# Kernel optimization log

Measured on AMD Instinct MI355X. Metric: run time of the kernel, lower is better.

## Reference

```python
import jax, jax.numpy as jnp
import numpy as np

V, E, HD, B, L, T = 50000, 512, 1024, 64, 512, 16
H = HD // 2
START, STOP = 14, 15
NEG = -10000.0


def setup_inputs() -> dict:
    key = jax.random.key(0)
    ks = jax.random.split(key, 14)
    def n(k, shape, s=0.1):
        return jax.random.normal(k, shape, dtype=jnp.float32) * s
    sentences = jax.random.randint(ks[0], (B, L), 0, V)
    embed = n(ks[1], (V, E), 1.0)
    Wih_f = n(ks[2], (4 * H, E)); Whh_f = n(ks[3], (4 * H, H)); b_f = n(ks[4], (4 * H,))
    Wih_b = n(ks[5], (4 * H, E)); Whh_b = n(ks[6], (4 * H, H)); b_b = n(ks[7], (4 * H,))
    h0 = n(ks[8], (2, B, H), 1.0)  # torch init_hidden uses randn
    c0 = n(ks[9], (2, B, H), 1.0)
    W_tag = n(ks[10], (T, HD)); b_tag = n(ks[11], (T,))
    transitions = jax.random.normal(ks[12], (T, T), dtype=jnp.float32)
    transitions = transitions.at[START, :].set(NEG).at[:, STOP].set(NEG)
    return dict(sentences=sentences, embed=embed, Wih_f=Wih_f, Whh_f=Whh_f, b_f=b_f,
                Wih_b=Wih_b, Whh_b=Whh_b, b_b=b_b, h0=h0, c0=c0,
                W_tag=W_tag, b_tag=b_tag, transitions=transitions)


def _lstm_dir(x, h0, c0, Wih, Whh, b, reverse):
    # x: [L, B, E]; torch gate order i, f, g, o
    def step(carry, xt):
        h, c = carry
        g = xt @ Wih.T + h @ Whh.T + b  # [B, 4H]
        i, f, gg, o = jnp.split(g, 4, axis=-1)
        c = jax.nn.sigmoid(f) * c + jax.nn.sigmoid(i) * jnp.tanh(gg)
        h = jax.nn.sigmoid(o) * jnp.tanh(c)
        return (h, c), h
    _, hs = jax.lax.scan(step, (h0, c0), x, reverse=reverse)
    return hs  # [L, B, H], outputs in original time order


def _viterbi(feats, transitions):
    # feats: [L, T]. Vectorized tag recurrence: fuse matrix-broadcast + max/argmax per step.
    init = jnp.full((T,), NEG, dtype=feats.dtype).at[START].set(0.0)
    def step(fv, feat):
        scores = fv[None, :] + transitions  # [next_tag, prev_tag]
        return jnp.max(scores, axis=1) + feat, jnp.argmax(scores, axis=1)
    fv, bps = jax.lax.scan(step, init, feats)
    term = fv + transitions[STOP]
    best = jnp.argmax(term)
    def back(tag, bp):
        return bp[tag], tag
    _, path = jax.lax.scan(back, best, bps, reverse=True)
    return term[best], path


def reference(sentences, embed, Wih_f, Whh_f, b_f, Wih_b, Whh_b, b_b, h0, c0, W_tag, b_tag, transitions):
    x = embed[sentences]                      # [B, L, E]
    xt = jnp.transpose(x, (1, 0, 2))          # [L, B, E]
    hf = _lstm_dir(xt, h0[0], c0[0], Wih_f, Whh_f, b_f, False)
    hb = _lstm_dir(xt, h0[1], c0[1], Wih_b, Whh_b, b_b, True)
    hs = jnp.concatenate([hf, hb], axis=-1)   # [L, B, HD]
    feats = jnp.einsum('lbh,th->lbt', hs, W_tag) + b_tag  # [L, B, T]
    feats = jnp.transpose(feats, (1, 0, 2))   # [B, L, T]
    scores, paths = jax.vmap(lambda f: _viterbi(f, transitions))(feats)
    return scores, paths
```

## Files before the change

kernel.cpp:

```cpp
#include <hip/hip_runtime.h>
#include <cstddef>

#define LL 512
#define BB 64
#define EE 512
#define HH 512
#define TT 16
#define START_TAG 14
#define STOP_TAG 15
#define NBLK_DIR 64u

__device__ __forceinline__ unsigned short f2bf(float f) {
  unsigned u = __builtin_bit_cast(unsigned, f);
  unsigned r = u + 0x7FFFu + ((u >> 16) & 1u);
  return (unsigned short)(r >> 16);
}

template <typename XT> __device__ __forceinline__ float ldx(const XT* p);
template <> __device__ __forceinline__ float ldx<float>(const float* p) { return *p; }
template <> __device__ __forceinline__ float ldx<unsigned short>(const unsigned short* p) {
  return __builtin_bit_cast(float, (unsigned)(*p) << 16);
}
template <typename XT> __device__ __forceinline__ void stx(XT* p, float v);
template <> __device__ __forceinline__ void stx<float>(float* p, float v) { *p = v; }
template <> __device__ __forceinline__ void stx<unsigned short>(unsigned short* p, float v) { *p = f2bf(v); }

#define AP 132

template <typename XT>
__global__ __launch_bounds__(256) void gemm_xp(
    const int* __restrict__ sent, const float* __restrict__ embed,
    const float* __restrict__ Wf, const float* __restrict__ Wb,
    const float* __restrict__ bf, const float* __restrict__ bb,
    XT* __restrict__ XPf, XT* __restrict__ XPb)
{
  __shared__ float Al[16 * AP];
  __shared__ float Bl[16 * AP];
  __shared__ int tok[128];

  const int bid = blockIdx.x;
  const int mt = bid & 255;
  const int nt = bid >> 8;
  const int m0 = mt << 7;
  const int n0g = nt << 7;
  const int dir = n0g >> 11;
  const int n0 = n0g & 2047;
  const float* W = dir ? Wb : Wf;
  const float* bias = dir ? bb : bf;
  XT* XP = dir ? XPb : XPf;
  const int tid = threadIdx.x;

  if (tid < 128) {
    int m = m0 + tid;
    int l = m >> 6, b = m & 63;
    tok[tid] = sent[b * LL + l];
  }
  __syncthreads();

  float acc[8][8];
#pragma unroll
  for (int i = 0; i < 8; ++i)
#pragma unroll
    for (int j = 0; j < 8; ++j) acc[i][j] = 0.f;

  const int ty = tid >> 4, tx = tid & 15;

#pragma unroll 1
  for (int k0 = 0; k0 < EE; k0 += 16) {
    __syncthreads();
    for (int i = tid; i < 512; i += 256) {
      int row = i >> 2, q = i & 3;
      float4 va = *(const float4*)(embed + (size_t)tok[row] * EE + k0 + q * 4);
      Al[(q * 4 + 0) * AP + row] = va.x;
      Al[(q * 4 + 1) * AP + row] = va.y;
      Al[(q * 4 + 2) * AP + row] = va.z;
      Al[(q * 4 + 3) * AP + row] = va.w;
      float4 vb = *(const float4*)(W + (size_t)(n0 + row) * EE + k0 + q * 4);
      Bl[(q * 4 + 0) * AP + row] = vb.x;
      Bl[(q * 4 + 1) * AP + row] = vb.y;
      Bl[(q * 4 + 2) * AP + row] = vb.z;
      Bl[(q * 4 + 3) * AP + row] = vb.w;
    }
    __syncthreads();
#pragma unroll
    for (int kk = 0; kk < 16; ++kk) {
      float4 a0 = *(const float4*)(Al + kk * AP + ty * 8);
      float4 a1 = *(const float4*)(Al + kk * AP + ty * 8 + 4);
      float4 b0 = *(const float4*)(Bl + kk * AP + tx * 8);
      float4 b1 = *(const float4*)(Bl + kk * AP + tx * 8 + 4);
      float av[8] = {a0.x, a0.y, a0.z, a0.w, a1.x, a1.y, a1.z, a1.w};
      float bv[8] = {b0.x, b0.y, b0.z, b0.w, b1.x, b1.y, b1.z, b1.w};
#pragma unroll
      for (int i = 0; i < 8; ++i)
#pragma unroll
        for (int j = 0; j < 8; ++j) acc[i][j] = fmaf(av[i], bv[j], acc[i][j]);
    }
  }

  float bval[8];
#pragma unroll
  for (int j = 0; j < 8; ++j) bval[j] = bias[n0 + tx * 8 + j];

#pragma unroll
  for (int i = 0; i < 8; ++i) {
    const int m = m0 + ty * 8 + i;
    const int t = m >> 6, b = m & 63;
#pragma unroll
    for (int j = 0; j < 8; ++j) {
      const int n = n0 + tx * 8 + j;
      const int col = n & 511, g = n >> 9;
      stx<XT>(XP + (((size_t)t * HH + col) * 4 + g) * BB + b, acc[i][j] + bval[j]);
    }
  }
}

__device__ __forceinline__ void dir_barrier(unsigned* cnt, unsigned* rel,
                                            unsigned phase) {
  __syncthreads();
  if (threadIdx.x == 0) {
    __threadfence();
    unsigned old = __hip_atomic_fetch_add(cnt, 1u, __ATOMIC_RELAXED,
                                          __HIP_MEMORY_SCOPE_AGENT);
    if (old == phase * NBLK_DIR - 1u) {
      __hip_atomic_store(rel, phase, __ATOMIC_RELEASE, __HIP_MEMORY_SCOPE_AGENT);
    } else {
      while (__hip_atomic_load(rel, __ATOMIC_ACQUIRE, __HIP_MEMORY_SCOPE_AGENT) < phase)
        __builtin_amdgcn_s_sleep(2);
    }
    __threadfence();
  }
  __syncthreads();
}

template <typename XT>
__global__ __launch_bounds__(512) void lstm_rec(
    const XT* __restrict__ XPTf, const XT* __restrict__ XPTb,
    const float* __restrict__ Whh_f, const float* __restrict__ Whh_b,
    const float* __restrict__ h0, const float* __restrict__ c0,
    float* __restrict__ hbuf,
    float* __restrict__ hs,
    unsigned* __restrict__ bar)
{
  const int bid = blockIdx.x;
  const int dir = bid >> 6;
  const int blk = bid & 63;
  const int tid = threadIdx.x;
  const int wv = __builtin_amdgcn_readfirstlane(tid >> 6);
  const int lane = tid & 63;
  const int col = (blk << 3) + wv;

  const float* Whh = dir ? Whh_b : Whh_f;
  const XT* XP = dir ? XPTb : XPTf;
  float* hA = hbuf + (size_t)dir * (2 * HH * BB);
  float* hB = hA + HH * BB;
  unsigned* cnt = bar + (dir ? 32 : 0);
  unsigned* rel = bar + (dir ? 96 : 64);

  const float* W0 = Whh + ((size_t)0 * HH + col) * HH;
  const float* W1 = Whh + ((size_t)1 * HH + col) * HH;
  const float* W2 = Whh + ((size_t)2 * HH + col) * HH;
  const float* W3 = Whh + ((size_t)3 * HH + col) * HH;

  float creg = c0[(size_t)dir * BB * HH + (size_t)lane * HH + col];
  hA[col * BB + lane] = h0[(size_t)dir * BB * HH + (size_t)lane * HH + col];

  unsigned phase = 1;
  dir_barrier(cnt, rel, phase++);

#pragma unroll 1
  for (int step = 0; step < LL; ++step) {
    const int t = dir ? (LL - 1 - step) : step;
    const float* hcur = (step & 1) ? hB : hA;
    float* hnxt = (step & 1) ? hA : hB;

    const XT* xpp = XP + ((size_t)t * HH + col) * 4 * BB + lane;
    const float xp0 = ldx<XT>(xpp);
    const float xp1 = ldx<XT>(xpp + BB);
    const float xp2 = ldx<XT>(xpp + 2 * BB);
    const float xp3 = ldx<XT>(xpp + 3 * BB);

    float a0 = 0.f, a1 = 0.f, a2 = 0.f, a3 = 0.f;
#pragma unroll 4
    for (int k4 = 0; k4 < HH; k4 += 4) {
      const float4 w0 = *(const float4*)(W0 + k4);
      const float4 w1 = *(const float4*)(W1 + k4);
      const float4 w2 = *(const float4*)(W2 + k4);
      const float4 w3 = *(const float4*)(W3 + k4);
      const float hk0 = hcur[(k4 + 0) * BB + lane];
      const float hk1 = hcur[(k4 + 1) * BB + lane];
      const float hk2 = hcur[(k4 + 2) * BB + lane];
      const float hk3 = hcur[(k4 + 3) * BB + lane];
      a0 = fmaf(hk0, w0.x, a0); a1 = fmaf(hk0, w1.x, a1);
      a2 = fmaf(hk0, w2.x, a2); a3 = fmaf(hk0, w3.x, a3);
      a0 = fmaf(hk1, w0.y, a0); a1 = fmaf(hk1, w1.y, a1);
      a2 = fmaf(hk1, w2.y, a2); a3 = fmaf(hk1, w3.y, a3);
      a0 = fmaf(hk2, w0.z, a0); a1 = fmaf(hk2, w1.z, a1);
      a2 = fmaf(hk2, w2.z, a2); a3 = fmaf(hk2, w3.z, a3);
      a0 = fmaf(hk3, w0.w, a0); a1 = fmaf(hk3, w1.w, a1);
      a2 = fmaf(hk3, w2.w, a2); a3 = fmaf(hk3, w3.w, a3);
    }

    const float ig = 1.f / (1.f + expf(-(xp0 + a0)));
    const float fg = 1.f / (1.f + expf(-(xp1 + a1)));
    const float gg = tanhf(xp2 + a2);
    const float og = 1.f / (1.f + expf(-(xp3 + a3)));
    creg = fg * creg + ig * gg;
    const float hv = og * tanhf(creg);

    hnxt[col * BB + lane] = hv;
    hs[((size_t)t * BB + lane) * 1024 + dir * HH + col] = hv;

    dir_barrier(cnt, rel, phase++);
  }
}

__global__ __launch_bounds__(64) void feats_k(
    const float* __restrict__ hs, const float* __restrict__ Wt,
    const float* __restrict__ bt, float* __restrict__ feats)
{
  const int bid = blockIdx.x;
  const int l = bid >> 6, b = bid & 63;
  const int tid = threadIdx.x;
  const int tag = tid & 15, q = tid >> 4;
  const float* hrow = hs + ((size_t)l * BB + b) * 1024;
  const float* wrow = Wt + tag * 1024;
  float p = 0.f;
#pragma unroll 4
  for (int i = 0; i < 64; ++i) {
    int k = q * 256 + i * 4;
    float4 h4 = *(const float4*)(hrow + k);
    float4 w4 = *(const float4*)(wrow + k);
    p += h4.x * w4.x + h4.y * w4.y + h4.z * w4.z + h4.w * w4.w;
  }
  p += __shfl_xor(p, 16);
  p += __shfl_xor(p, 32);
  if (q == 0) feats[((size_t)b * LL + l) * TT + tag] = p + bt[tag];
}

__global__ __launch_bounds__(64) void viterbi_k(
    const float* __restrict__ feats, const float* __restrict__ trans,
    float* __restrict__ out)
{
  __shared__ float fv[TT];
  __shared__ unsigned char bps[LL * TT];
  const int b = blockIdx.x;
  const int tid = threadIdx.x;

  float trow[16];
  if (tid < 16) {
#pragma unroll
    for (int p = 0; p < 16; ++p) trow[p] = trans[tid * TT + p];
    fv[tid] = (tid == START_TAG) ? 0.f : -10000.f;
  }
  __syncthreads();

  const float* fb = feats + (size_t)b * LL * TT;
#pragma unroll 1
  for (int t = 0; t < LL; ++t) {
    float best = 0.f; int barg = 0;
    if (tid < 16) {
      best = fv[0] + trow[0]; barg = 0;
#pragma unroll
      for (int p = 1; p < 16; ++p) {
        float s = fv[p] + trow[p];
        if (s > best) { best = s; barg = p; }
      }
      bps[t * TT + tid] = (unsigned char)barg;
    }
    __syncthreads();
    if (tid < 16) fv[tid] = best + fb[t * TT + tid];
    __syncthreads();
  }

  if (tid == 0) {
    float bsc = fv[0] + trans[STOP_TAG * TT + 0];
    int btag = 0;
#pragma unroll
    for (int j = 1; j < 16; ++j) {
      float s = fv[j] + trans[STOP_TAG * TT + j];
      if (s > bsc) { bsc = s; btag = j; }
    }
    out[b] = bsc;
    int tg = btag;
    for (int t = LL - 1; t >= 0; --t) {
      out[BB + b * LL + t] = (float)tg;
      tg = bps[t * TT + tg];
    }
  }
}

template <typename XT>
static void run_pipeline(const int* sent, const float* embed,
                         const float* Wih_f, const float* Whh_f, const float* b_f,
                         const float* Wih_b, const float* Whh_b, const float* b_b,
                         const float* h0, const float* c0,
                         const float* Wt, const float* bt, const float* trans,
                         float* out, char* wsb, hipStream_t stream)
{
  const size_t XPE = (size_t)LL * HH * 4 * BB;
  XT* XPTf = (XT*)(wsb + 1024);
  XT* XPTb = XPTf + XPE;
  char* after_xp = (char*)(XPTb + XPE);
  float* hbuf = (float*)after_xp;
  float* hs = (float*)(after_xp + 2 * 2 * HH * BB * 4);
  float* feats = (float*)((char*)hs + (size_t)LL * BB * 1024 * 4);
  unsigned* bar = (unsigned*)wsb;

  hipMemsetAsync(wsb, 0, 1024, stream);

  hipLaunchKernelGGL((gemm_xp<XT>), dim3(8192), dim3(256), 0, stream,
                     sent, embed, Wih_f, Wih_b, b_f, b_b, XPTf, XPTb);

  void* ka[9];
  ka[0] = (void*)&XPTf; ka[1] = (void*)&XPTb;
  ka[2] = (void*)&Whh_f; ka[3] = (void*)&Whh_b;
  ka[4] = (void*)&h0;  ka[5] = (void*)&c0;
  ka[6] = (void*)&hbuf; ka[7] = (void*)&hs; ka[8] = (void*)&bar;
  hipLaunchCooperativeKernel((void*)(lstm_rec<XT>), dim3(128), dim3(512),
                             ka, 0, stream);

  hipLaunchKernelGGL(feats_k, dim3(32768), dim3(64), 0, stream, hs, Wt, bt, feats);
  hipLaunchKernelGGL(viterbi_k, dim3(64), dim3(64), 0, stream, feats, trans, out);
}

extern "C" void kernel_launch(void* const* d_in, const int* in_sizes, int n_in,
                              void* d_out, int out_size, void* d_ws, size_t ws_size,
                              hipStream_t stream)
{
  (void)in_sizes; (void)n_in; (void)out_size;
  const int* sent = (const int*)d_in[0];
  const float* embed = (const float*)d_in[1];
  const float* Wih_f = (const float*)d_in[2];
  const float* Whh_f = (const float*)d_in[3];
  const float* b_f = (const float*)d_in[4];
  const float* Wih_b = (const float*)d_in[5];
  const float* Whh_b = (const float*)d_in[6];
  const float* b_b = (const float*)d_in[7];
  const float* h0 = (const float*)d_in[8];
  const float* c0 = (const float*)d_in[9];
  const float* Wt = (const float*)d_in[10];
  const float* bt = (const float*)d_in[11];
  const float* trans = (const float*)d_in[12];
  float* out = (float*)d_out;

  const size_t XPE = (size_t)LL * HH * 4 * BB;
  const size_t FIXED = 1024 + 2ull * 2 * HH * BB * 4
                     + (size_t)LL * BB * 1024 * 4
                     + (size_t)BB * LL * TT * 4;
  const size_t needA = FIXED + 2 * XPE * 4;
  const size_t needB = FIXED + 2 * XPE * 2;

  char* wsb = (char*)d_ws;
  if (ws_size >= needA) {
    run_pipeline<float>(sent, embed, Wih_f, Whh_f, b_f, Wih_b, Whh_b, b_b,
                        h0, c0, Wt, bt, trans, out, wsb, stream);
  } else if (ws_size >= needB) {
    run_pipeline<unsigned short>(sent, embed, Wih_f, Whh_f, b_f, Wih_b, Whh_b, b_b,
                                 h0, c0, Wt, bt, trans, out, wsb, stream);
  }
}
```

Baseline: 16.18 ms.

## Split LSTM recurrence across 256 blocks with bf16 hidden state staged in LDS

The persistent recurrent kernel now uses 128 blocks per direction, each owning 4 hidden columns. Each block's 8 waves split the K dimension in half and reduce the two partial sums through shared memory. The hidden state is stored as bf16 in a paired layout, copied into LDS at every step, and read back as packed 32-bit words. The input projection is always bf16 and the spin-wait sleep is shortened. This spreads each step's matvec over more CUs and cuts hidden-state traffic, at the cost of more blocks in the grid barrier, extra __syncthreads, a 64KB LDS copy per step, and bf16 rounding of h in the recurrence.

```diff
diff --git a/kernel.cpp b/kernel.cpp
--- a/kernel.cpp
+++ b/kernel.cpp
@@ -8,31 +8,27 @@
 #define TT 16
 #define START_TAG 14
 #define STOP_TAG 15
-#define NBLK_DIR 64u
-
-__device__ __forceinline__ unsigned short f2bf(float f) {
-  unsigned u = __builtin_bit_cast(unsigned, f);
-  unsigned r = u + 0x7FFFu + ((u >> 16) & 1u);
-  return (unsigned short)(r >> 16);
-}
-
-template <typename XT> __device__ __forceinline__ float ldx(const XT* p);
-template <> __device__ __forceinline__ float ldx<float>(const float* p) { return *p; }
-template <> __device__ __forceinline__ float ldx<unsigned short>(const unsigned short* p) {
-  return __builtin_bit_cast(float, (unsigned)(*p) << 16);
-}
-template <typename XT> __device__ __forceinline__ void stx(XT* p, float v);
-template <> __device__ __forceinline__ void stx<float>(float* p, float v) { *p = v; }
-template <> __device__ __forceinline__ void stx<unsigned short>(unsigned short* p, float v) { *p = f2bf(v); }
+#define NBLK_DIR 128u
+
+typedef unsigned short u16;
+typedef unsigned int u32;
+
+__device__ __forceinline__ u16 f2bf(float f) {
+  u32 u = __builtin_bit_cast(u32, f);
+  u32 r = u + 0x7FFFu + ((u >> 16) & 1u);
+  return (u16)(r >> 16);
+}
+__device__ __forceinline__ float bf2f(u16 h) {
+  return __builtin_bit_cast(float, (u32)h << 16);
+}
 
 #define AP 132
 
-template <typename XT>
 __global__ __launch_bounds__(256) void gemm_xp(
     const int* __restrict__ sent, const float* __restrict__ embed,
     const float* __restrict__ Wf, const float* __restrict__ Wb,
     const float* __restrict__ bf, const float* __restrict__ bb,
-    XT* __restrict__ XPf, XT* __restrict__ XPb)
+    u16* __restrict__ XPf, u16* __restrict__ XPb)
 {
   __shared__ float Al[16 * AP];
   __shared__ float Bl[16 * AP];
@@ -47,7 +43,7 @@
   const int n0 = n0g & 2047;
   const float* W = dir ? Wb : Wf;
   const float* bias = dir ? bb : bf;
-  XT* XP = dir ? XPb : XPf;
+  u16* XP = dir ? XPb : XPf;
   const int tid = threadIdx.x;
 
   if (tid < 128) {
@@ -109,7 +105,7 @@
     for (int j = 0; j < 8; ++j) {
       const int n = n0 + tx * 8 + j;
       const int col = n & 511, g = n >> 9;
-      stx<XT>(XP + (((size_t)t * HH + col) * 4 + g) * BB + b, acc[i][j] + bval[j]);
+      XP[(((size_t)t * HH + col) * 4 + g) * BB + b] = f2bf(acc[i][j] + bval[j]);
     }
   }
 }
@@ -125,44 +121,53 @@
       __hip_atomic_store(rel, phase, __ATOMIC_RELEASE, __HIP_MEMORY_SCOPE_AGENT);
     } else {
       while (__hip_atomic_load(rel, __ATOMIC_ACQUIRE, __HIP_MEMORY_SCOPE_AGENT) < phase)
-        __builtin_amdgcn_s_sleep(2);
+        __builtin_amdgcn_s_sleep(1);
     }
     __threadfence();
   }
   __syncthreads();
 }
 
-template <typename XT>
 __global__ __launch_bounds__(512) void lstm_rec(
-    const XT* __restrict__ XPTf, const XT* __restrict__ XPTb,
+    const u16* __restrict__ XPTf, const u16* __restrict__ XPTb,
     const float* __restrict__ Whh_f, const float* __restrict__ Whh_b,
     const float* __restrict__ h0, const float* __restrict__ c0,
-    float* __restrict__ hbuf,
+    u16* __restrict__ hbuf,
     float* __restrict__ hs,
     unsigned* __restrict__ bar)
 {
+  extern __shared__ u32 ldsH[];
+  float4* part = (float4*)ldsH;
+
   const int bid = blockIdx.x;
-  const int dir = bid >> 6;
-  const int blk = bid & 63;
+  const int dir = bid >> 7;
+  const int cblk = bid & 127;
+  const int c0col = cblk << 2;
   const int tid = threadIdx.x;
   const int wv = __builtin_amdgcn_readfirstlane(tid >> 6);
   const int lane = tid & 63;
-  const int col = (blk << 3) + wv;
+  const int mycol = c0col + (wv & 3);
+  const int khalf = wv >> 2;
 
   const float* Whh = dir ? Whh_b : Whh_f;
-  const XT* XP = dir ? XPTb : XPTf;
-  float* hA = hbuf + (size_t)dir * (2 * HH * BB);
-  float* hB = hA + HH * BB;
+  const u16* XP = dir ? XPTb : XPTf;
+  u16* hA = hbuf + (size_t)dir * 2 * HH * BB;
+  u16* hB = hA + HH * BB;
   unsigned* cnt = bar + (dir ? 32 : 0);
   unsigned* rel = bar + (dir ? 96 : 64);
 
-  const float* W0 = Whh + ((size_t)0 * HH + col) * HH;
-  const float* W1 = Whh + ((size_t)1 * HH + col) * HH;
-  const float* W2 = Whh + ((size_t)2 * HH + col) * HH;
-  const float* W3 = Whh + ((size_t)3 * HH + col) * HH;
-
-  float creg = c0[(size_t)dir * BB * HH + (size_t)lane * HH + col];
-  hA[col * BB + lane] = h0[(size_t)dir * BB * HH + (size_t)lane * HH + col];
+  const float4* W0 = (const float4*)(Whh + ((size_t)0 * HH + mycol) * HH + khalf * 256);
+  const float4* W1 = (const float4*)(Whh + ((size_t)1 * HH + mycol) * HH + khalf * 256);
+  const float4* W2 = (const float4*)(Whh + ((size_t)2 * HH + mycol) * HH + khalf * 256);
+  const float4* W3 = (const float4*)(Whh + ((size_t)3 * HH + mycol) * HH + khalf * 256);
+
+  float creg = 0.f;
+  if (tid < 256) {
+    const int ucol = c0col + (tid >> 6), b = tid & 63;
+    creg = c0[(size_t)dir * BB * HH + (size_t)b * HH + ucol];
+    const float hv0 = h0[(size_t)dir * BB * HH + (size_t)b * HH + ucol];
+    hA[(ucol >> 1) * 128 + b * 2 + (ucol & 1)] = f2bf(hv0);
+  }
 
   unsigned phase = 1;
   dir_barrier(cnt, rel, phase++);
@@ -170,45 +175,74 @@
 #pragma unroll 1
   for (int step = 0; step < LL; ++step) {
     const int t = dir ? (LL - 1 - step) : step;
-    const float* hcur = (step & 1) ? hB : hA;
-    float* hnxt = (step & 1) ? hA : hB;
-
-    const XT* xpp = XP + ((size_t)t * HH + col) * 4 * BB + lane;
-    const float xp0 = ldx<XT>(xpp);
-    const float xp1 = ldx<XT>(xpp + BB);
-    const float xp2 = ldx<XT>(xpp + 2 * BB);
-    const float xp3 = ldx<XT>(xpp + 3 * BB);
+    const u16* hcur = (step & 1) ? hB : hA;
+    u16* hnxt = (step & 1) ? hA : hB;
+
+    {
+      const uint4* src = (const uint4*)hcur;
+#pragma unroll
+      for (int i = 0; i < 8; ++i) {
+        ((uint4*)ldsH)[i * 512 + tid] = src[i * 512 + tid];
+      }
+    }
+    __syncthreads();
+
+    float xp0 = 0.f, xp1 = 0.f, xp2 = 0.f, xp3 = 0.f;
+    if (tid < 256) {
+      const int ucol = c0col + (tid >> 6), b = tid & 63;
+      const u16* xpp = XP + ((size_t)t * HH + ucol) * 4 * BB + b;
+      xp0 = bf2f(xpp[0]);
+      xp1 = bf2f(xpp[BB]);
+      xp2 = bf2f(xpp[2 * BB]);
+      xp3 = bf2f(xpp[3 * BB]);
+    }
 
     float a0 = 0.f, a1 = 0.f, a2 = 0.f, a3 = 0.f;
-#pragma unroll 4
-    for (int k4 = 0; k4 < HH; k4 += 4) {
-      const float4 w0 = *(const float4*)(W0 + k4);
-      const float4 w1 = *(const float4*)(W1 + k4);
-      const float4 w2 = *(const float4*)(W2 + k4);
-      const float4 w3 = *(const float4*)(W3 + k4);
-      const float hk0 = hcur[(k4 + 0) * BB + lane];
-      const float hk1 = hcur[(k4 + 1) * BB + lane];
-      const float hk2 = hcur[(k4 + 2) * BB + lane];
-      const float hk3 = hcur[(k4 + 3) * BB + lane];
-      a0 = fmaf(hk0, w0.x, a0); a1 = fmaf(hk0, w1.x, a1);
-      a2 = fmaf(hk0, w2.x, a2); a3 = fmaf(hk0, w3.x, a3);
-      a0 = fmaf(hk1, w0.y, a0); a1 = fmaf(hk1, w1.y, a1);
-      a2 = fmaf(hk1, w2.y, a2); a3 = fmaf(hk1, w3.y, a3);
-      a0 = fmaf(hk2, w0.z, a0); a1 = fmaf(hk2, w1.z, a1);
-      a2 = fmaf(hk2, w2.z, a2); a3 = fmaf(hk2, w3.z, a3);
-      a0 = fmaf(hk3, w0.w, a0); a1 = fmaf(hk3, w1.w, a1);
-      a2 = fmaf(hk3, w2.w, a2); a3 = fmaf(hk3, w3.w, a3);
-    }
-
-    const float ig = 1.f / (1.f + expf(-(xp0 + a0)));
-    const float fg = 1.f / (1.f + expf(-(xp1 + a1)));
-    const float gg = tanhf(xp2 + a2);
-    const float og = 1.f / (1.f + expf(-(xp3 + a3)));
-    creg = fg * creg + ig * gg;
-    const float hv = og * tanhf(creg);
-
-    hnxt[col * BB + lane] = hv;
-    hs[((size_t)t * BB + lane) * 1024 + dir * HH + col] = hv;
+    const u32* hp = ldsH + khalf * 8192;
+#pragma unroll 8
+    for (int p = 0; p < 128; p += 2) {
+      const u32 v0 = hp[p * 64 + lane];
+      const u32 v1 = hp[(p + 1) * 64 + lane];
+      const float4 w0 = W0[p >> 1];
+      const float4 w1 = W1[p >> 1];
+      const float4 w2 = W2[p >> 1];
+      const float4 w3 = W3[p >> 1];
+      const float h0f = __builtin_bit_cast(float, v0 << 16);
+      const float h1f = __builtin_bit_cast(float, v0 & 0xFFFF0000u);
+      const float h2f = __builtin_bit_cast(float, v1 << 16);
+      const float h3f = __builtin_bit_cast(float, v1 & 0xFFFF0000u);
+      a0 = fmaf(h0f, w0.x, a0); a1 = fmaf(h0f, w1.x, a1);
+      a2 = fmaf(h0f, w2.x, a2); a3 = fmaf(h0f, w3.x, a3);
+      a0 = fmaf(h1f, w0.y, a0); a1 = fmaf(h1f, w1.y, a1);
+      a2 = fmaf(h1f, w2.y, a2); a3 = fmaf(h1f, w3.y, a3);
+      a0 = fmaf(h2f, w0.z, a0); a1 = fmaf(h2f, w1.z, a1);
+      a2 = fmaf(h2f, w2.z, a2); a3 = fmaf(h2f, w3.z, a3);
+      a0 = fmaf(h3f, w0.w, a0); a1 = fmaf(h3f, w1.w, a1);
+      a2 = fmaf(h3f, w2.w, a2); a3 = fmaf(h3f, w3.w, a3);
+    }
+
+    __syncthreads();
+    if (wv >= 4) {
+      part[(wv - 4) * 64 + lane] = make_float4(a0, a1, a2, a3);
+    }
+    __syncthreads();
+
+    if (tid < 256) {
+      const int ucol = c0col + (tid >> 6), b = tid & 63;
+      const float4 o = part[wv * 64 + lane];
+      const float g0 = a0 + o.x + xp0;
+      const float g1 = a1 + o.y + xp1;
+      const float g2 = a2 + o.z + xp2;
+      const float g3 = a3 + o.w + xp3;
+      const float ig = 1.f / (1.f + expf(-g0));
+      const float fg = 1.f / (1.f + expf(-g1));
+      const float gg = tanhf(g2);
+      const float og = 1.f / (1.f + expf(-g3));
+      creg = fg * creg + ig * gg;
+      const float hv = og * tanhf(creg);
+      hnxt[(ucol >> 1) * 128 + b * 2 + (ucol & 1)] = f2bf(hv);
+      hs[((size_t)t * BB + b) * 1024 + dir * HH + ucol] = hv;
+    }
 
     dir_barrier(cnt, rel, phase++);
   }
@@ -287,40 +321,6 @@
       tg = bps[t * TT + tg];
     }
   }
-}
-
-template <typename XT>
-static void run_pipeline(const int* sent, const float* embed,
-                         const float* Wih_f, const float* Whh_f, const float* b_f,
-                         const float* Wih_b, const float* Whh_b, const float* b_b,
-                         const float* h0, const float* c0,
-                         const float* Wt, const float* bt, const float* trans,
-                         float* out, char* wsb, hipStream_t stream)
-{
-  const size_t XPE = (size_t)LL * HH * 4 * BB;
-  XT* XPTf = (XT*)(wsb + 1024);
-  XT* XPTb = XPTf + XPE;
-  char* after_xp = (char*)(XPTb + XPE);
-  float* hbuf = (float*)after_xp;
-  float* hs = (float*)(after_xp + 2 * 2 * HH * BB * 4);
-  float* feats = (float*)((char*)hs + (size_t)LL * BB * 1024 * 4);
-  unsigned* bar = (unsigned*)wsb;
-
-  hipMemsetAsync(wsb, 0, 1024, stream);
-
-  hipLaunchKernelGGL((gemm_xp<XT>), dim3(8192), dim3(256), 0, stream,
-                     sent, embed, Wih_f, Wih_b, b_f, b_b, XPTf, XPTb);
-
-  void* ka[9];
-  ka[0] = (void*)&XPTf; ka[1] = (void*)&XPTb;
-  ka[2] = (void*)&Whh_f; ka[3] = (void*)&Whh_b;
-  ka[4] = (void*)&h0;  ka[5] = (void*)&c0;
-  ka[6] = (void*)&hbuf; ka[7] = (void*)&hs; ka[8] = (void*)&bar;
-  hipLaunchCooperativeKernel((void*)(lstm_rec<XT>), dim3(128), dim3(512),
-                             ka, 0, stream);
-
-  hipLaunchKernelGGL(feats_k, dim3(32768), dim3(64), 0, stream, hs, Wt, bt, feats);
-  hipLaunchKernelGGL(viterbi_k, dim3(64), dim3(64), 0, stream, feats, trans, out);
 }
 
 extern "C" void kernel_launch(void* const* d_in, const int* in_sizes, int n_in,
@@ -344,18 +344,35 @@
   float* out = (float*)d_out;
 
   const size_t XPE = (size_t)LL * HH * 4 * BB;
-  const size_t FIXED = 1024 + 2ull * 2 * HH * BB * 4
-                     + (size_t)LL * BB * 1024 * 4
-                     + (size_t)BB * LL * TT * 4;
-  const size_t needA = FIXED + 2 * XPE * 4;
-  const size_t needB = FIXED + 2 * XPE * 2;
+  const size_t XP_B = XPE * 2;
+  const size_t HBUF_B = 2ull * 2 * HH * BB * 2;
+  const size_t HS_B = (size_t)LL * BB * 1024 * 4;
+  const size_t FEATS_B = (size_t)BB * LL * TT * 4;
+  const size_t need = 1024 + 2 * XP_B + HBUF_B + HS_B + FEATS_B;
+
+  if (ws_size < need) return;
 
   char* wsb = (char*)d_ws;
-  if (ws_size >= needA) {
-    run_pipeline<float>(sent, embed, Wih_f, Whh_f, b_f, Wih_b, Whh_b, b_b,
-                        h0, c0, Wt, bt, trans, out, wsb, stream);
-  } else if (ws_size >= needB) {
-    run_pipeline<unsigned short>(sent, embed, Wih_f, Whh_f, b_f, Wih_b, Whh_b, b_b,
-                                 h0, c0, Wt, bt, trans, out, wsb, stream);
-  }
-}
+  unsigned* bar = (unsigned*)wsb;
+  u16* XPTf = (u16*)(wsb + 1024);
+  u16* XPTb = (u16*)(wsb + 1024 + XP_B);
+  u16* hbuf = (u16*)(wsb + 1024 + 2 * XP_B);
+  float* hs = (float*)(wsb + 1024 + 2 * XP_B + HBUF_B);
+  float* feats = (float*)(wsb + 1024 + 2 * XP_B + HBUF_B + HS_B);
+
+  hipMemsetAsync(wsb, 0, 1024, stream);
+
+  hipLaunchKernelGGL(gemm_xp, dim3(8192), dim3(256), 0, stream,
+                     sent, embed, Wih_f, Wih_b, b_f, b_b, XPTf, XPTb);
+
+  void* ka[9];
+  ka[0] = (void*)&XPTf; ka[1] = (void*)&XPTb;
+  ka[2] = (void*)&Whh_f; ka[3] = (void*)&Whh_b;
+  ka[4] = (void*)&h0;  ka[5] = (void*)&c0;
+  ka[6] = (void*)&hbuf; ka[7] = (void*)&hs; ka[8] = (void*)&bar;
+  hipLaunchCooperativeKernel((void*)lstm_rec, dim3(256), dim3(512),
+                             ka, 65536, stream);
+
+  hipLaunchKernelGGL(feats_k, dim3(32768), dim3(64), 0, stream, hs, Wt, bt, feats);
+  hipLaunchKernelGGL(viterbi_k, dim3(64), dim3(64), 0, stream, feats, trans, out);
+}
```

Result: slower. 20.01 ms (+23.6%).
